# Performance work log

Hardware: AMD Instinct MI355X
Metric: run time of the kernel (lower is better)

## Reference

```python
import jax, jax.numpy as jnp
from jax import lax
import numpy as np

COEFF_INIT = 0.04


def setup_inputs() -> dict:
    key = jax.random.key(0)
    k1, _ = jax.random.split(key)
    B, C, T = 16, 80, 16000
    x = jax.random.normal(k1, (B, C, T), dtype=jnp.float32)
    weights = jnp.ones((C,), dtype=jnp.float32) * COEFF_INIT
    return {"x": x, "weights": weights}


def reference(x, weights):
    # x: [B, C, T]; weights: [C] (per-channel EMA coefficient)
    w = jnp.clip(weights, 0.0, 1.0)  # [C]
    init = x[:, :, 0]                # [B, C]  (note: first step re-applies x0 -> output[...,0] == x0)
    xt = jnp.moveaxis(x, 2, 0)       # [T, B, C]

    def step(acc, xi):
        acc = w * xi + (1.0 - w) * acc
        return acc, acc

    _, ys = lax.scan(step, init, xt)  # ys: [T, B, C]
    return jnp.moveaxis(ys, 0, 2)     # [B, C, T]
```

## Files before the change

kernel.cpp:

```cpp
#include <hip/hip_runtime.h>

#define TPB 256
#define ROWLEN 16000
#define NROWS 1280
#define NCHUNK 250
#define SEGS 62
#define SCAN_OFF 16000

typedef float f32x4 __attribute__((ext_vector_type(4)));

__device__ __forceinline__ unsigned swz(unsigned s) { return s ^ ((s >> 4) & 7u); }

__global__ __launch_bounds__(TPB) void ema_kernel(const float* __restrict__ x,
                                                  const float* __restrict__ wts,
                                                  float* __restrict__ y) {
  __shared__ float lds[16256];
  const int row  = blockIdx.x;
  const int c    = row % 80;
  const int tid  = threadIdx.x;
  const int lane = tid & 63;
  const int wv   = tid >> 6;

  const float* __restrict__ xr = x + (size_t)row * ROWLEN;
  float* __restrict__ yr       = y + (size_t)row * ROWLEN;

  float w = wts[c];
  w = fminf(fmaxf(w, 0.f), 1.f);
  const float d = 1.f - w;

  for (int seg = wv; seg < SEGS; seg += 4) {
    unsigned p = (unsigned)(seg * 64 + lane);
    unsigned g = swz(p);
    __builtin_amdgcn_global_load_lds(
        (const __attribute__((address_space(1))) void*)(xr + g * 4),
        (__attribute__((address_space(3))) void*)(&lds[seg * 256]),
        16, 0, 0);
  }
  if (tid < 128) {
    int wrd = 15872 + tid;
    unsigned p = swz((unsigned)(wrd >> 2));
    lds[p * 4 + (wrd & 3)] = xr[wrd];
  }
  __syncthreads();

  const float init = lds[0];

  f32x4 xv[16];
  float L = 0.f;
  if (tid < NCHUNK) {
#pragma unroll
    for (int k = 0; k < 16; ++k) {
      unsigned p = swz((unsigned)(tid * 16 + k));
      xv[k] = *(const f32x4*)&lds[p * 4];
    }
#pragma unroll
    for (int k = 0; k < 16; ++k)
#pragma unroll
      for (int j = 0; j < 4; ++j)
        L = w * xv[k][j] + d * L;
  }
  float D = d * d; D = D * D; D = D * D; D = D * D; D = D * D; D = D * D;

  float* S = &lds[SCAN_OFF];
  float s = (tid < NCHUNK) ? L : 0.f;
  S[tid] = s;
  __syncthreads();
  float Dp = D;
  for (int step = 1; step < TPB; step <<= 1) {
    float add = (tid >= step) ? S[tid - step] : 0.f;
    __syncthreads();
    s = s + Dp * add;
    S[tid] = s;
    Dp = Dp * Dp;
    __syncthreads();
  }

  if (tid < NCHUNK) {
    float acc = powf(D, (float)tid) * init;
    if (tid > 0) acc += S[tid - 1];
#pragma unroll
    for (int k = 0; k < 16; ++k) {
      f32x4 yv;
#pragma unroll
      for (int j = 0; j < 4; ++j) {
        acc = w * xv[k][j] + d * acc;
        yv[j] = acc;
      }
      unsigned p = swz((unsigned)(tid * 16 + k));
      *(f32x4*)&lds[p * 4] = yv;
    }
  }
  __syncthreads();

  for (int seg = wv; seg < SEGS; seg += 4) {
    unsigned p = (unsigned)(seg * 64 + lane);
    unsigned g = swz(p);
    f32x4 v = *(const f32x4*)&lds[p * 4];
    *(f32x4*)(yr + g * 4) = v;
  }
  if (tid < 128) {
    int wrd = 15872 + tid;
    unsigned p = swz((unsigned)(wrd >> 2));
    yr[wrd] = lds[p * 4 + (wrd & 3)];
  }
}

extern "C" void kernel_launch(void* const* d_in, const int* in_sizes, int n_in,
                              void* d_out, int out_size, void* d_ws, size_t ws_size,
                              hipStream_t stream) {
  const float* x   = (const float*)d_in[0];
  const float* wts = (const float*)d_in[1];
  float* y         = (float*)d_out;
  ema_kernel<<<NROWS, TPB, 0, stream>>>(x, wts, y);
}
```

Before: 34.15 us.

## Drop LDS staging and load/store row chunks directly from global memory

Removes the swizzled LDS staging buffer and the async global-to-LDS copy. Each thread now reads its 256-byte chunk straight from global memory into registers and writes its results back directly. This saves two LDS passes and two barriers and cuts LDS use from about 64KB to 1KB per block, so more blocks can be resident. The cost is uncoalesced access: adjacent lanes touch addresses 256 bytes apart, which may waste memory bandwidth.

```diff
diff --git a/kernel.cpp b/kernel.cpp
--- a/kernel.cpp
+++ b/kernel.cpp
@@ -4,22 +4,16 @@
 #define ROWLEN 16000
 #define NROWS 1280
 #define NCHUNK 250
-#define SEGS 62
-#define SCAN_OFF 16000
 
 typedef float f32x4 __attribute__((ext_vector_type(4)));
-
-__device__ __forceinline__ unsigned swz(unsigned s) { return s ^ ((s >> 4) & 7u); }
 
 __global__ __launch_bounds__(TPB) void ema_kernel(const float* __restrict__ x,
                                                   const float* __restrict__ wts,
                                                   float* __restrict__ y) {
-  __shared__ float lds[16256];
-  const int row  = blockIdx.x;
-  const int c    = row % 80;
-  const int tid  = threadIdx.x;
-  const int lane = tid & 63;
-  const int wv   = tid >> 6;
+  __shared__ float S[TPB];
+  const int row = blockIdx.x;
+  const int c   = row % 80;
+  const int tid = threadIdx.x;
 
   const float* __restrict__ xr = x + (size_t)row * ROWLEN;
   float* __restrict__ yr       = y + (size_t)row * ROWLEN;
@@ -28,40 +22,22 @@
   w = fminf(fmaxf(w, 0.f), 1.f);
   const float d = 1.f - w;
 
-  for (int seg = wv; seg < SEGS; seg += 4) {
-    unsigned p = (unsigned)(seg * 64 + lane);
-    unsigned g = swz(p);
-    __builtin_amdgcn_global_load_lds(
-        (const __attribute__((address_space(1))) void*)(xr + g * 4),
-        (__attribute__((address_space(3))) void*)(&lds[seg * 256]),
-        16, 0, 0);
-  }
-  if (tid < 128) {
-    int wrd = 15872 + tid;
-    unsigned p = swz((unsigned)(wrd >> 2));
-    lds[p * 4 + (wrd & 3)] = xr[wrd];
-  }
-  __syncthreads();
-
-  const float init = lds[0];
-
   f32x4 xv[16];
   float L = 0.f;
   if (tid < NCHUNK) {
+    const f32x4* __restrict__ src = (const f32x4*)xr + (size_t)tid * 16;
 #pragma unroll
-    for (int k = 0; k < 16; ++k) {
-      unsigned p = swz((unsigned)(tid * 16 + k));
-      xv[k] = *(const f32x4*)&lds[p * 4];
-    }
+    for (int k = 0; k < 16; ++k) xv[k] = src[k];
 #pragma unroll
     for (int k = 0; k < 16; ++k)
 #pragma unroll
       for (int j = 0; j < 4; ++j)
         L = w * xv[k][j] + d * L;
   }
+  const float init = xr[0];
+
   float D = d * d; D = D * D; D = D * D; D = D * D; D = D * D; D = D * D;
 
-  float* S = &lds[SCAN_OFF];
   float s = (tid < NCHUNK) ? L : 0.f;
   S[tid] = s;
   __syncthreads();
@@ -78,6 +54,7 @@
   if (tid < NCHUNK) {
     float acc = powf(D, (float)tid) * init;
     if (tid > 0) acc += S[tid - 1];
+    f32x4* __restrict__ dst = (f32x4*)yr + (size_t)tid * 16;
 #pragma unroll
     for (int k = 0; k < 16; ++k) {
       f32x4 yv;
@@ -86,22 +63,8 @@
         acc = w * xv[k][j] + d * acc;
         yv[j] = acc;
       }
-      unsigned p = swz((unsigned)(tid * 16 + k));
-      *(f32x4*)&lds[p * 4] = yv;
+      dst[k] = yv;
     }
-  }
-  __syncthreads();
-
-  for (int seg = wv; seg < SEGS; seg += 4) {
-    unsigned p = (unsigned)(seg * 64 + lane);
-    unsigned g = swz(p);
-    f32x4 v = *(const f32x4*)&lds[p * 4];
-    *(f32x4*)(yr + g * 4) = v;
-  }
-  if (tid < 128) {
-    int wrd = 15872 + tid;
-    unsigned p = swz((unsigned)(wrd >> 2));
-    yr[wrd] = lds[p * 4 + (wrd & 3)];
   }
 }
 
```

After: 49.57 us. 45.2% more time.
